# Kernel optimization log

Measured on AMD Instinct MI355X. Metric: run time of the kernel, lower is better.

Reference implementation:

```python
import jax, jax.numpy as jnp
import numpy as np

P = 5.0
A = 10.0
NUM_VARS = 1_000_000
NUM_CLAUSES = 1_000_000
E = 3_000_000  # edges per polarity


def setup_inputs() -> dict:
    key = jax.random.key(0)
    k1, k2, k3, k4, k5 = jax.random.split(key, 5)
    xv = jax.random.uniform(k1, (NUM_VARS, 1), dtype=jnp.float32)
    # clause rows: shuffled arange % NUM_CLAUSES so every clause is non-empty
    cp = jax.random.permutation(k2, jnp.arange(E, dtype=jnp.int64) % NUM_CLAUSES)
    cn = jax.random.permutation(k3, jnp.arange(E, dtype=jnp.int64) % NUM_CLAUSES)
    vp = jax.random.randint(k4, (E,), 0, NUM_VARS, dtype=jnp.int64)
    vn = jax.random.randint(k5, (E,), 0, NUM_VARS, dtype=jnp.int64)
    adj_pos = jnp.stack([cp, vp])  # [2, E]
    adj_neg = jnp.stack([cn, vn])  # [2, E]
    clause_count = jnp.ones((NUM_CLAUSES,), dtype=jnp.float32)
    return {"xv": xv, "adj_pos": adj_pos, "adj_neg": adj_neg, "clause_count": clause_count}


def reference(xv, adj_pos, adj_neg, clause_count):
    x = xv.reshape(-1)            # [V]
    xn = 1.0 - x
    # gather literal values and their exp(p*.) weights along edges
    lit = jnp.concatenate([x[adj_pos[1]], xn[adj_neg[1]]])            # [2E]
    xe = jnp.concatenate([jnp.exp(P * x)[adj_pos[1]], jnp.exp(P * xn)[adj_neg[1]]])  # [2E]
    idx = jnp.concatenate([adj_pos[0], adj_neg[0]])                   # [2E]
    numerator = jax.ops.segment_sum(lit * xe, idx, num_segments=NUM_CLAUSES)
    dominator = jax.ops.segment_sum(xe, idx, num_segments=NUM_CLAUSES)
    # push_to_side: 1/(1+exp(a*(0.5-x))) == sigmoid(a*(x-0.5))
    sm = jax.nn.sigmoid(A * (numerator / dominator - 0.5))            # [NUM_CLAUSES]
    # metric = mse_loss(sm, clause_count)
    loss = jnp.mean((sm - clause_count) ** 2)
    return loss
```

## Files before the change

kernel.cpp:

```cpp
#include <hip/hip_runtime.h>

constexpr int   NUM_CLAUSES = 1000000;
constexpr int   NUM_EDGES   = 3000000;
constexpr float Pc = 5.0f;
constexpr float Ac = 10.0f;

constexpr float FXSCALE = 64.0f;
constexpr float FXINV   = 1.0f / 64.0f;

constexpr int NB  = 250;
constexpr int CPB = 4000;
constexpr int CAP = CPB * 6;

constexpr int TPB   = 512;
constexpr int RPB   = 8192;
constexpr int RPT   = RPB / TPB;
constexpr int NBLKP = (NUM_EDGES + RPB - 1) / RPB;

constexpr float QSCALE = 1048575.0f;
constexpr float QINV   = 1.0f / 1048575.0f;

constexpr size_t OFF_CTR = 24000000;
constexpr size_t OFF_PAR = 24001024;

__device__ __forceinline__ unsigned pack_fx(float num, float den) {
    unsigned lo = (unsigned)(num * FXSCALE + 0.5f);
    unsigned hi = (unsigned)(den * FXSCALE + 0.5f);
    return lo | (hi << 16);
}

__global__ __launch_bounds__(TPB)
void partition_kernel(const int*   __restrict__ adj_pos,
                      const int*   __restrict__ adj_neg,
                      const float* __restrict__ x,
                      unsigned* __restrict__ recs,
                      unsigned* __restrict__ counters) {
    __shared__ unsigned      hist[NB];
    __shared__ unsigned      sbase[NB];
    __shared__ unsigned      lbase[NB];
    __shared__ unsigned      srec[RPB];
    __shared__ unsigned char sbid[RPB];
    __shared__ unsigned      wsum[TPB / 64];
    __shared__ unsigned      woff[TPB / 64];

    const bool neg   = (blockIdx.x >= (unsigned)NBLKP);
    const int  sblk  = neg ? (int)blockIdx.x - NBLKP : (int)blockIdx.x;
    const int  start = sblk * RPB;
    const int  n     = min(RPB, NUM_EDGES - start);
    const int* crow  = neg ? adj_neg : adj_pos;
    const int* vrow  = crow + NUM_EDGES;
    const int  tid   = (int)threadIdx.x;

    for (int b = tid; b < NB; b += TPB) hist[b] = 0;
    __syncthreads();

    int cc_[RPT], vv_[RPT];
    if (n == RPB) {
        #pragma unroll
        for (int j = 0; j < RPT / 4; ++j) {
            int4 c4 = ((const int4*)(crow + start))[j * TPB + tid];
            int4 v4 = ((const int4*)(vrow + start))[j * TPB + tid];
            cc_[4*j] = c4.x; cc_[4*j+1] = c4.y; cc_[4*j+2] = c4.z; cc_[4*j+3] = c4.w;
            vv_[4*j] = v4.x; vv_[4*j+1] = v4.y; vv_[4*j+2] = v4.z; vv_[4*j+3] = v4.w;
        }
    } else {
        #pragma unroll
        for (int r = 0; r < RPT; ++r) {
            int pos = 4 * ((r >> 2) * TPB + tid) + (r & 3);
            cc_[r] = (pos < n) ? crow[start + pos] : -1;
            vv_[r] = (pos < n) ? vrow[start + pos] : 0;
        }
    }

    float xv[RPT];
    #pragma unroll
    for (int r = 0; r < RPT; ++r) xv[r] = x[vv_[r]];

    unsigned rec[RPT], meta[RPT];
    #pragma unroll
    for (int r = 0; r < RPT; ++r) {
        meta[r] = 0xFFFFFFFFu;
        if (cc_[r] >= 0) {
            int   c   = cc_[r];
            int   b   = c / CPB;
            float lit = neg ? (1.0f - xv[r]) : xv[r];
            unsigned q = (unsigned)(lit * QSCALE + 0.5f);
            rec[r] = (q << 12) | (unsigned)(c - b * CPB);
            unsigned rank = atomicAdd(&hist[b], 1u);
            meta[r] = ((unsigned)b << 13) | rank;
        }
    }
    __syncthreads();

    unsigned h    = (tid < NB) ? hist[tid] : 0u;
    unsigned incl = h;
    #pragma unroll
    for (int off = 1; off < 64; off <<= 1) {
        unsigned t = __shfl_up(incl, off, 64);
        if ((tid & 63) >= off) incl += t;
    }
    if ((tid & 63) == 63) wsum[tid >> 6] = incl;
    __syncthreads();
    if (tid == 0) {
        unsigned a = 0;
        #pragma unroll
        for (int w = 0; w < TPB / 64; ++w) { woff[w] = a; a += wsum[w]; }
    }
    __syncthreads();
    if (tid < NB) {
        lbase[tid] = incl - h + woff[tid >> 6];
        sbase[tid] = h ? atomicAdd(&counters[tid], h) : 0u;
    }
    __syncthreads();

    #pragma unroll
    for (int r = 0; r < RPT; ++r) {
        if (meta[r] != 0xFFFFFFFFu) {
            unsigned b    = meta[r] >> 13;
            unsigned rank = meta[r] & 0x1FFFu;
            unsigned p    = lbase[b] + rank;
            srec[p] = rec[r];
            sbid[p] = (unsigned char)b;
        }
    }
    __syncthreads();

    for (int p = tid; p < n; p += TPB) {
        unsigned b = sbid[p];
        recs[(size_t)b * CAP + sbase[b] + ((unsigned)p - lbase[b])] = srec[p];
    }
}

__global__ __launch_bounds__(1024)
void bucket_loss_kernel(const uint4* __restrict__ recs4,
                        const float* __restrict__ cc,
                        float* __restrict__ partials) {
    __shared__ unsigned lacc[CPB];
    const int b = blockIdx.x;
    for (int j = threadIdx.x; j < CPB; j += 1024) lacc[j] = 0;
    __syncthreads();

    const uint4* r4 = recs4 + (size_t)b * (CAP / 4);
    for (int k = threadIdx.x; k < CAP / 4; k += 1024) {
        uint4 e = r4[k];
        #pragma unroll
        for (int k2 = 0; k2 < 4; ++k2) {
            unsigned r  = (&e.x)[k2];
            float lit = (float)(r >> 12) * QINV;
            float w   = __expf(Pc * lit);
            atomicAdd(&lacc[r & 0xFFFu], pack_fx(lit * w, w));
        }
    }
    __syncthreads();

    float v = 0.0f;
    const float* gc = cc + (size_t)b * CPB;
    for (int j = threadIdx.x; j < CPB; j += 1024) {
        unsigned a   = lacc[j];
        float    num = (float)(a & 0xffffu) * FXINV;
        float    den = (float)(a >> 16)     * FXINV;
        float    sm  = 1.0f / (1.0f + __expf(-Ac * (num / den - 0.5f)));
        float    e0  = sm - gc[j];
        v += e0 * e0;
    }
    v *= 1.0f / (float)NUM_CLAUSES;

    #pragma unroll
    for (int off = 32; off > 0; off >>= 1)
        v += __shfl_down(v, off, 64);

    __shared__ float partial[16];
    int lane = threadIdx.x & 63;
    int wid  = threadIdx.x >> 6;
    if (lane == 0) partial[wid] = v;
    __syncthreads();
    if (threadIdx.x == 0) {
        float s = 0.f;
        #pragma unroll
        for (int w = 0; w < 16; ++w) s += partial[w];
        partials[b] = s;
    }
}

__global__ void final_kernel(const float* __restrict__ partials,
                             float* __restrict__ out, int n) {
    float v = 0.0f;
    for (int i = threadIdx.x; i < n; i += 256) v += partials[i];

    #pragma unroll
    for (int off = 32; off > 0; off >>= 1)
        v += __shfl_down(v, off, 64);

    __shared__ float partial[4];
    int lane = threadIdx.x & 63;
    int wid  = threadIdx.x >> 6;
    if (lane == 0) partial[wid] = v;
    __syncthreads();
    if (threadIdx.x == 0)
        out[0] = partial[0] + partial[1] + partial[2] + partial[3];
}

extern "C" void kernel_launch(void* const* d_in, const int* in_sizes, int n_in,
                              void* d_out, int out_size, void* d_ws, size_t ws_size,
                              hipStream_t stream) {
    const float* xv      = (const float*)d_in[0];
    const int*   adj_pos = (const int*)  d_in[1];
    const int*   adj_neg = (const int*)  d_in[2];
    const float* cc      = (const float*)d_in[3];

    char* ws = (char*)d_ws;
    unsigned* recs     = (unsigned*)ws;
    unsigned* counters = (unsigned*)(ws + OFF_CTR);
    float*    partials = (float*)   (ws + OFF_PAR);
    float*    out      = (float*)d_out;

    hipMemsetAsync(counters, 0, NB * sizeof(unsigned), stream);

    partition_kernel<<<2 * NBLKP, TPB, 0, stream>>>(adj_pos, adj_neg, xv,
                                                    recs, counters);

    bucket_loss_kernel<<<NB, 1024, 0, stream>>>((const uint4*)recs, cc, partials);

    final_kernel<<<1, 256, 0, stream>>>(partials, out, NB);
}
```

Before: 145.2 us.

## Replace global bucket scatter with per-block sorted runs plus offset table

The partition kernel now writes each block's locally bucket-sorted records contiguously to its own slot, together with a per-block table of bucket start offsets. This replaces the global atomic counters, the memset and the scattered writes into fixed-capacity bucket arrays. The loss kernel then has each wavefront walk every partition block's run for its bucket using the offset table. This removes scattered global writes and the counter atomics, but the reads in the loss kernel become many short, irregular segments, and each bucket block must read 734 table entries.

```diff
diff --git a/kernel.cpp b/kernel.cpp
--- a/kernel.cpp
+++ b/kernel.cpp
@@ -10,18 +10,19 @@
 
 constexpr int NB  = 250;
 constexpr int CPB = 4000;
-constexpr int CAP = CPB * 6;
 
 constexpr int TPB   = 512;
 constexpr int RPB   = 8192;
 constexpr int RPT   = RPB / TPB;
 constexpr int NBLKP = (NUM_EDGES + RPB - 1) / RPB;
+constexpr int NBLK  = 2 * NBLKP;
+constexpr int TW    = NB + 1;
 
 constexpr float QSCALE = 1048575.0f;
 constexpr float QINV   = 1.0f / 1048575.0f;
 
-constexpr size_t OFF_CTR = 24000000;
-constexpr size_t OFF_PAR = 24001024;
+constexpr size_t OFF_TAB = (size_t)NBLK * RPB * sizeof(unsigned);
+constexpr size_t OFF_PAR = OFF_TAB + (size_t)NBLK * TW * sizeof(unsigned);
 
 __device__ __forceinline__ unsigned pack_fx(float num, float den) {
     unsigned lo = (unsigned)(num * FXSCALE + 0.5f);
@@ -34,17 +35,16 @@
                       const int*   __restrict__ adj_neg,
                       const float* __restrict__ x,
                       unsigned* __restrict__ recs,
-                      unsigned* __restrict__ counters) {
-    __shared__ unsigned      hist[NB];
-    __shared__ unsigned      sbase[NB];
-    __shared__ unsigned      lbase[NB];
-    __shared__ unsigned      srec[RPB];
-    __shared__ unsigned char sbid[RPB];
-    __shared__ unsigned      wsum[TPB / 64];
-    __shared__ unsigned      woff[TPB / 64];
-
-    const bool neg   = (blockIdx.x >= (unsigned)NBLKP);
-    const int  sblk  = neg ? (int)blockIdx.x - NBLKP : (int)blockIdx.x;
+                      unsigned* __restrict__ tab) {
+    __shared__ unsigned hist[NB];
+    __shared__ unsigned lbase[TW];
+    __shared__ unsigned srec[RPB];
+    __shared__ unsigned wsum[TPB / 64];
+    __shared__ unsigned woff[TPB / 64];
+
+    const int  g     = (int)blockIdx.x;
+    const bool neg   = (g >= NBLKP);
+    const int  sblk  = neg ? g - NBLKP : g;
     const int  start = sblk * RPB;
     const int  n     = min(RPB, NUM_EDGES - start);
     const int* crow  = neg ? adj_neg : adj_pos;
@@ -107,10 +107,8 @@
         for (int w = 0; w < TPB / 64; ++w) { woff[w] = a; a += wsum[w]; }
     }
     __syncthreads();
-    if (tid < NB) {
-        lbase[tid] = incl - h + woff[tid >> 6];
-        sbase[tid] = h ? atomicAdd(&counters[tid], h) : 0u;
-    }
+    if (tid < NB) lbase[tid] = incl - h + woff[tid >> 6];
+    if (tid == 0) lbase[NB] = (unsigned)n;
     __syncthreads();
 
     #pragma unroll
@@ -118,36 +116,39 @@
         if (meta[r] != 0xFFFFFFFFu) {
             unsigned b    = meta[r] >> 13;
             unsigned rank = meta[r] & 0x1FFFu;
-            unsigned p    = lbase[b] + rank;
-            srec[p] = rec[r];
-            sbid[p] = (unsigned char)b;
-        }
-    }
-    __syncthreads();
-
-    for (int p = tid; p < n; p += TPB) {
-        unsigned b = sbid[p];
-        recs[(size_t)b * CAP + sbase[b] + ((unsigned)p - lbase[b])] = srec[p];
-    }
+            srec[lbase[b] + rank] = rec[r];
+        }
+    }
+    __syncthreads();
+
+    unsigned* gout = recs + (size_t)g * RPB;
+    for (int p = tid; p < n; p += TPB) gout[p] = srec[p];
+    unsigned* trow = tab + (size_t)g * TW;
+    for (int b = tid; b < TW; b += TPB) trow[b] = lbase[b];
 }
 
 __global__ __launch_bounds__(1024)
-void bucket_loss_kernel(const uint4* __restrict__ recs4,
+void bucket_loss_kernel(const unsigned* __restrict__ recs,
+                        const unsigned* __restrict__ tab,
                         const float* __restrict__ cc,
                         float* __restrict__ partials) {
     __shared__ unsigned lacc[CPB];
-    const int b = blockIdx.x;
+    const int b    = (int)blockIdx.x;
+    const int lane = (int)threadIdx.x & 63;
+    const int wid  = (int)threadIdx.x >> 6;
+
     for (int j = threadIdx.x; j < CPB; j += 1024) lacc[j] = 0;
     __syncthreads();
 
-    const uint4* r4 = recs4 + (size_t)b * (CAP / 4);
-    for (int k = threadIdx.x; k < CAP / 4; k += 1024) {
-        uint4 e = r4[k];
-        #pragma unroll
-        for (int k2 = 0; k2 < 4; ++k2) {
-            unsigned r  = (&e.x)[k2];
-            float lit = (float)(r >> 12) * QINV;
-            float w   = __expf(Pc * lit);
+    for (int blk = wid; blk < NBLK; blk += 16) {
+        const unsigned* trow = tab + (size_t)blk * TW + b;
+        unsigned s = trow[0];
+        unsigned e = trow[1];
+        const unsigned* rr = recs + (size_t)blk * RPB;
+        for (unsigned k = s + (unsigned)lane; k < e; k += 64) {
+            unsigned r   = rr[k];
+            float    lit = (float)(r >> 12) * QINV;
+            float    w   = __expf(Pc * lit);
             atomicAdd(&lacc[r & 0xFFFu], pack_fx(lit * w, w));
         }
     }
@@ -170,8 +171,6 @@
         v += __shfl_down(v, off, 64);
 
     __shared__ float partial[16];
-    int lane = threadIdx.x & 63;
-    int wid  = threadIdx.x >> 6;
     if (lane == 0) partial[wid] = v;
     __syncthreads();
     if (threadIdx.x == 0) {
@@ -210,16 +209,13 @@
 
     char* ws = (char*)d_ws;
     unsigned* recs     = (unsigned*)ws;
-    unsigned* counters = (unsigned*)(ws + OFF_CTR);
+    unsigned* tab      = (unsigned*)(ws + OFF_TAB);
     float*    partials = (float*)   (ws + OFF_PAR);
     float*    out      = (float*)d_out;
 
-    hipMemsetAsync(counters, 0, NB * sizeof(unsigned), stream);
-
-    partition_kernel<<<2 * NBLKP, TPB, 0, stream>>>(adj_pos, adj_neg, xv,
-                                                    recs, counters);
-
-    bucket_loss_kernel<<<NB, 1024, 0, stream>>>((const uint4*)recs, cc, partials);
+    partition_kernel<<<NBLK, TPB, 0, stream>>>(adj_pos, adj_neg, xv, recs, tab);
+
+    bucket_loss_kernel<<<NB, 1024, 0, stream>>>(recs, tab, cc, partials);
 
     final_kernel<<<1, 256, 0, stream>>>(partials, out, NB);
 }
```

After: 158.8 us. +9.4%, slower.
